# Kernel optimization log

Hardware: AMD Instinct MI355X
Metric: run time of the kernel (lower is better)

The kernel has to match this reference:

```python
import jax, jax.numpy as jnp
import numpy as np

N = 100000  # nodes per type (user, tweet)
E = 500000  # edges per relation
D = 128     # input feature dim
H = 128     # hidden dim


def _seg_mean(h_src, src, dst, n_dst):
    # DGL copy_u + mean: mean of source features over incoming edges; zero for in-degree 0.
    msg = h_src[src]                                                    # [E, F] gather
    s = jax.ops.segment_sum(msg, dst, num_segments=n_dst)               # [n_dst, F] scatter-add
    cnt = jax.ops.segment_sum(jnp.ones((src.shape[0], 1), h_src.dtype), dst, num_segments=n_dst)
    return s / jnp.maximum(cnt, 1.0)


def setup_inputs() -> dict:
    key = jax.random.key(0)
    ks = jax.random.split(key, 24)
    f = lambda i, shp, s=1.0: jax.random.normal(ks[i], shp, dtype=jnp.float32) * s
    return {
        'x_user': f(0, (N, D)), 'x_tweet': f(1, (N, D)),
        # layer 1, relation 'posts' (user -> tweet) and 'posted_by' (tweet -> user)
        'w1ps': f(2, (H, D), 0.05), 'b1ps': f(3, (H,), 0.05),
        'w1pn': f(4, (H, D), 0.05), 'b1pn': f(5, (H,), 0.05),
        'w1bs': f(6, (H, D), 0.05), 'b1bs': f(7, (H,), 0.05),
        'w1bn': f(8, (H, D), 0.05), 'b1bn': f(9, (H,), 0.05),
        # layer 2 (out_feats = 1, no activation)
        'w2ps': f(10, (1, H), 0.05), 'b2ps': f(11, (1,), 0.05),
        'w2pn': f(12, (1, H), 0.05), 'b2pn': f(13, (1,), 0.05),
        'w2bs': f(14, (1, H), 0.05), 'b2bs': f(15, (1,), 0.05),
        'w2bn': f(16, (1, H), 0.05), 'b2bn': f(17, (1,), 0.05),
        'src_posts': jax.random.randint(ks[18], (E,), 0, N),
        'dst_posts': jax.random.randint(ks[19], (E,), 0, N),
        'src_pb': jax.random.randint(ks[20], (E,), 0, N),
        'dst_pb': jax.random.randint(ks[21], (E,), 0, N),
    }


def reference(x_user, x_tweet,
              w1ps, b1ps, w1pn, b1pn, w1bs, b1bs, w1bn, b1bn,
              w2ps, b2ps, w2pn, b2pn, w2bs, b2bs, w2bn, b2bn,
              src_posts, dst_posts, src_pb, dst_pb):
    # ---- conv1: DivFeatConv per relation, relu, cross-relation sum (one rel per dst type) ----
    neigh_t = _seg_mean(x_user, src_posts, dst_posts, N)               # user -posts-> tweet
    h_tweet = jax.nn.relu(x_tweet @ w1ps.T + b1ps + neigh_t @ w1pn.T + b1pn)
    neigh_u = _seg_mean(x_tweet, src_pb, dst_pb, N)                    # tweet -posted_by-> user
    h_user = jax.nn.relu(x_user @ w1bs.T + b1bs + neigh_u @ w1bn.T + b1bn)
    # ---- conv2: out_feats=1, identity activation ----
    neigh_t2 = _seg_mean(h_user, src_posts, dst_posts, N)
    out_tweet = h_tweet @ w2ps.T + b2ps + neigh_t2 @ w2pn.T + b2pn     # [N, 1]
    neigh_u2 = _seg_mean(h_tweet, src_pb, dst_pb, N)
    out_user = h_user @ w2bs.T + b2bs + neigh_u2 @ w2bn.T + b2bn       # [N, 1]
    return (out_user, out_tweet)
```

## Files before the change

kernel.cpp:

```cpp
#include <hip/hip_runtime.h>

#define N_NODES 100000
#define N_EDGES 500000
#define DIM 128
#define GB_E 1954
#define GB_EI 489
#define GB_N 391
#define GB_CVT 12500
#define GB_G 782
#define GB_SEG 6250

typedef __attribute__((ext_vector_type(8))) short short8;
typedef __attribute__((ext_vector_type(4))) float f32x4;

__device__ __forceinline__ ushort f2bf(float f) {
    unsigned u = __float_as_uint(f);
    u += 0x7FFF + ((u >> 16) & 1);
    return (ushort)(u >> 16);
}
__device__ __forceinline__ float bf2f(ushort s) {
    return __uint_as_float(((unsigned)s) << 16);
}


__device__ __forceinline__ void build_body(const int* __restrict__ src,
                                           const int* __restrict__ dst,
                                           int* __restrict__ head,
                                           int2* __restrict__ entry, int bid) {
    int e = bid * 256 + threadIdx.x;
    if (e < N_EDGES) {
        int d = dst[e];
        int old = atomicExch(&head[d], e);
        entry[e] = make_int2(src[e], old);
    }
}

__device__ __forceinline__ void build_body_ilp(const int* __restrict__ src,
                                               const int* __restrict__ dst,
                                               int* __restrict__ head,
                                               int2* __restrict__ entry, int bid) {
    int base = bid * 1024 + threadIdx.x;
    int e[4], d[4], s[4], old[4];
    bool ok[4];
#pragma unroll
    for (int k = 0; k < 4; ++k) {
        e[k] = base + k * 256;
        ok[k] = (e[k] < N_EDGES);
        d[k] = ok[k] ? dst[e[k]] : 0;
        s[k] = ok[k] ? src[e[k]] : 0;
    }
#pragma unroll
    for (int k = 0; k < 4; ++k)
        if (ok[k]) old[k] = atomicExch(&head[d[k]], e[k]);
#pragma unroll
    for (int k = 0; k < 4; ++k)
        if (ok[k]) entry[e[k]] = make_int2(s[k], old[k]);
}

__device__ __forceinline__ void cvt_body(const float* __restrict__ in,
                                         ushort* __restrict__ out, int bid) {
    int i = (bid * 256 + threadIdx.x) * 4;
    float4 v = *reinterpret_cast<const float4*>(&in[i]);
    ushort4 u = make_ushort4(f2bf(v.x), f2bf(v.y), f2bf(v.z), f2bf(v.w));
    *reinterpret_cast<ushort4*>(&out[i]) = u;
}

__device__ __forceinline__ void seg_body(const ushort* __restrict__ x,
                                         const int* __restrict__ head,
                                         const int2* __restrict__ entry,
                                         ushort* __restrict__ outbf, int bid) {
    int idx = bid * 256 + threadIdx.x;
    int node = idx >> 4;
    if (node >= N_NODES) return;
    int f = (idx & 15) << 3;
    float acc[8];
#pragma unroll
    for (int j = 0; j < 8; ++j) acc[j] = 0.f;
    int cnt = 0;
    int e = head[node];
    while (e >= 0) {
        int2 nd = entry[e];
        ++cnt;
        short8 v = *reinterpret_cast<const short8*>(&x[(size_t)nd.x * DIM + f]);
#pragma unroll
        for (int j = 0; j < 8; ++j) acc[j] += bf2f((ushort)v[j]);
        e = nd.y;
    }
    float r = 1.0f / fmaxf((float)cnt, 1.0f);
    union { ushort s[8]; uint4 v; } u;
#pragma unroll
    for (int j = 0; j < 8; ++j) u.s[j] = f2bf(acc[j] * r);
    *reinterpret_cast<uint4*>(&outbf[(size_t)node * DIM + f]) = u.v;
}

__device__ __forceinline__ float smean_body(const float* __restrict__ sval,
                                            const int* __restrict__ head,
                                            const int2* __restrict__ entry, int node) {
    float a = 0.f;
    int cnt = 0;
    int e = head[node];
    while (e >= 0) {
        int2 nd = entry[e];
        ++cnt;
        a += sval[nd.x];
        e = nd.y;
    }
    return a / fmaxf((float)cnt, 1.0f);
}

__device__ __forceinline__ void gemm_body(
    const ushort* __restrict__ Xsbf, const ushort* __restrict__ Nm,
    const ushort* __restrict__ Wsbf, const ushort* __restrict__ Wnbf,
    const float* __restrict__ bs, const float* __restrict__ bn,
    const float* __restrict__ w2a, const float* __restrict__ w2b,
    float* __restrict__ dself, float* __restrict__ dcross, int blk) {
    __shared__ ushort sA[128 * 64];
    __shared__ ushort sB[128 * 64];
    __shared__ float pS[2][2][128];

    const int tid = threadIdx.x;
    const int lane = tid & 63;
    const int wid = tid >> 6;
    const int wr = wid >> 1, wc = wid & 1;
    const int lr = lane & 15, lg = lane >> 4;
    const int row0 = blk * 128;

    f32x4 acc[4][4];
#pragma unroll
    for (int i = 0; i < 4; ++i)
#pragma unroll
        for (int j = 0; j < 4; ++j) acc[i][j] = (f32x4){0.f, 0.f, 0.f, 0.f};

    const int r = tid >> 1;
    const int hh = tid & 1;
    const int grow = row0 + r;
    const int swzr = (r & 7) << 4;

    for (int kb = 0; kb < 256; kb += 64) {
        const int kg = kb & 127;
        const bool self = (kb < 128);
        __syncthreads();
        {
            const uint4* g = reinterpret_cast<const uint4*>(self ? Xsbf : Nm);
#pragma unroll
            for (int q = 0; q < 4; ++q) {
                uint4 v = make_uint4(0, 0, 0, 0);
                if (grow < N_NODES)
                    v = g[((size_t)grow * DIM + kg + hh * 32 + q * 8) >> 3];
                int byte = (hh * 64 + q * 16) ^ swzr;
                *reinterpret_cast<uint4*>(&sA[r * 64 + (byte >> 1)]) = v;
            }
        }
        {
            const uint4* g = reinterpret_cast<const uint4*>(self ? Wsbf : Wnbf);
#pragma unroll
            for (int q = 0; q < 4; ++q) {
                uint4 v = g[(r * DIM + kg + hh * 32 + q * 8) >> 3];
                int byte = (hh * 64 + q * 16) ^ swzr;
                *reinterpret_cast<uint4*>(&sB[r * 64 + (byte >> 1)]) = v;
            }
        }
        __syncthreads();
#pragma unroll
        for (int ks = 0; ks < 2; ++ks) {
            short8 a[4], b[4];
#pragma unroll
            for (int fm = 0; fm < 4; ++fm) {
                int rr = wr * 64 + fm * 16 + lr;
                int byte = (ks * 64 + lg * 16) ^ ((rr & 7) << 4);
                a[fm] = *reinterpret_cast<const short8*>(&sA[rr * 64 + (byte >> 1)]);
            }
#pragma unroll
            for (int fn = 0; fn < 4; ++fn) {
                int cc = wc * 64 + fn * 16 + lr;
                int byte = (ks * 64 + lg * 16) ^ ((cc & 7) << 4);
                b[fn] = *reinterpret_cast<const short8*>(&sB[cc * 64 + (byte >> 1)]);
            }
#pragma unroll
            for (int fm = 0; fm < 4; ++fm)
#pragma unroll
                for (int fn = 0; fn < 4; ++fn)
                    acc[fm][fn] = __builtin_amdgcn_mfma_f32_16x16x32_bf16(
                        a[fm], b[fn], acc[fm][fn], 0, 0, 0);
        }
    }

    float bias[4], wa[4], wb[4];
#pragma unroll
    for (int fn = 0; fn < 4; ++fn) {
        int c = wc * 64 + fn * 16 + lr;
        bias[fn] = bs[c] + bn[c];
        wa[fn] = w2a[c];
        wb[fn] = w2b[c];
    }
#pragma unroll
    for (int fm = 0; fm < 4; ++fm) {
#pragma unroll
        for (int reg = 0; reg < 4; ++reg) {
            float pa = 0.f, pb = 0.f;
#pragma unroll
            for (int fn = 0; fn < 4; ++fn) {
                float h = fmaxf(acc[fm][fn][reg] + bias[fn], 0.f);
                pa = fmaf(h, wa[fn], pa);
                pb = fmaf(h, wb[fn], pb);
            }
#pragma unroll
            for (int m = 1; m < 16; m <<= 1) {
                pa += __shfl_xor(pa, m);
                pb += __shfl_xor(pb, m);
            }
            if (lr == 0) {
                int rloc = wr * 64 + fm * 16 + lg * 4 + reg;
                pS[wc][0][rloc] = pa;
                pS[wc][1][rloc] = pb;
            }
        }
    }
    __syncthreads();
    if (tid < 128) {
        int go = row0 + tid;
        if (go < N_NODES) {
            dself[go] = pS[0][0][tid] + pS[1][0][tid];
            dcross[go] = pS[0][1][tid] + pS[1][1][tid];
        }
    }
}


__global__ __launch_bounds__(256) void cvt_fat_kernel(
    const float* __restrict__ w0, const float* __restrict__ w1,
    const float* __restrict__ w2, const float* __restrict__ w3,
    ushort* __restrict__ o0, ushort* __restrict__ o1,
    ushort* __restrict__ o2, ushort* __restrict__ o3,
    const float* __restrict__ xu, const float* __restrict__ xt,
    ushort* __restrict__ xbf_u, ushort* __restrict__ xbf_t) {
    int bid = blockIdx.x;
    if (bid < 64) {
        int a = bid >> 4;
        const float* in = (a == 0) ? w0 : (a == 1) ? w1 : (a == 2) ? w2 : w3;
        ushort* out = (a == 0) ? o0 : (a == 1) ? o1 : (a == 2) ? o2 : o3;
        cvt_body(in, out, bid & 15);
    } else {
        int b = bid - 64;
        int which = (b >= GB_CVT);
        cvt_body(which ? xt : xu, which ? xbf_t : xbf_u, b - which * GB_CVT);
    }
}

__global__ __launch_bounds__(256) void build1_ilp_kernel(
    const int* __restrict__ src, const int* __restrict__ dst,
    int* __restrict__ head, int2* __restrict__ entry) {
    build_body_ilp(src, dst, head, entry, blockIdx.x);
}

__global__ __launch_bounds__(256) void seg_only_kernel(
    const ushort* __restrict__ x, const int* __restrict__ head,
    const int2* __restrict__ entry, ushort* __restrict__ outbf) {
    seg_body(x, head, entry, outbf, blockIdx.x);
}

__global__ __launch_bounds__(256) void fatG_kernel(
    const ushort* __restrict__ xbf_t, const ushort* __restrict__ nbf0,
    const ushort* __restrict__ wbf_ps, const ushort* __restrict__ wbf_pn,
    const float* __restrict__ b1ps, const float* __restrict__ b1pn,
    const float* __restrict__ w2ps, const float* __restrict__ w2bn,
    float* __restrict__ dself_t, float* __restrict__ scross_t,
    const int* __restrict__ s1, const int* __restrict__ d1,
    int* __restrict__ head_pb, int2* __restrict__ ent_pb) {
    int bid = blockIdx.x;
    if (bid < GB_G)
        gemm_body(xbf_t, nbf0, wbf_ps, wbf_pn, b1ps, b1pn, w2ps, w2bn,
                  dself_t, scross_t, bid);
    else
        build_body_ilp(s1, d1, head_pb, ent_pb, bid - GB_G);
}

__global__ __launch_bounds__(256) void fatC_kernel(
    const ushort* __restrict__ xbf_u, const ushort* __restrict__ nbf1,
    const ushort* __restrict__ wbf_bs, const ushort* __restrict__ wbf_bn,
    const float* __restrict__ b1bs, const float* __restrict__ b1bn,
    const float* __restrict__ w2bs, const float* __restrict__ w2pn,
    float* __restrict__ dself_u, float* __restrict__ scross_u,
    const float* __restrict__ scross_t,
    const int* __restrict__ head_pb, const int2* __restrict__ ent_pb,
    float* __restrict__ smean_u) {
    int bid = blockIdx.x;
    if (bid < GB_G) {
        gemm_body(xbf_u, nbf1, wbf_bs, wbf_bn, b1bs, b1bn, w2bs, w2pn,
                  dself_u, scross_u, bid);
    } else {
        int i = (bid - GB_G) * 256 + threadIdx.x;
        if (i < N_NODES) smean_u[i] = smean_body(scross_t, head_pb, ent_pb, i);
    }
}

__global__ __launch_bounds__(256) void tail_kernel(
    const float* __restrict__ dself_u, const float* __restrict__ smean_u,
    const float* __restrict__ dself_t, const float* __restrict__ scross_u,
    const int* __restrict__ head_posts, const int2* __restrict__ ent_posts,
    const float* __restrict__ b2bs, const float* __restrict__ b2bn,
    const float* __restrict__ b2ps, const float* __restrict__ b2pn,
    float* __restrict__ out) {
    int i = blockIdx.x * 256 + threadIdx.x;
    if (i >= N_NODES) return;
    out[N_NODES + i] = dself_t[i] + smean_body(scross_u, head_posts, ent_posts, i)
                       + b2ps[0] + b2pn[0];
    out[i] = dself_u[i] + smean_u[i] + b2bs[0] + b2bn[0];
}


__global__ __launch_bounds__(256) void cvtw_kernel(
    const float* __restrict__ w0, const float* __restrict__ w1,
    const float* __restrict__ w2, const float* __restrict__ w3,
    ushort* __restrict__ o0, ushort* __restrict__ o1,
    ushort* __restrict__ o2, ushort* __restrict__ o3) {
    int a = blockIdx.y;
    const float* in = (a == 0) ? w0 : (a == 1) ? w1 : (a == 2) ? w2 : w3;
    ushort* out = (a == 0) ? o0 : (a == 1) ? o1 : (a == 2) ? o2 : o3;
    cvt_body(in, out, blockIdx.x);
}

__global__ __launch_bounds__(256) void build_lists2_kernel(
    const int* __restrict__ s0, const int* __restrict__ d0,
    const int* __restrict__ s1, const int* __restrict__ d1,
    int* __restrict__ head2, int2* __restrict__ entry2) {
    const int rel = blockIdx.y;
    build_body(rel ? s1 : s0, rel ? d1 : d0, head2 + (size_t)rel * N_NODES,
               entry2 + (size_t)rel * N_EDGES, blockIdx.x);
}

__global__ __launch_bounds__(256) void seg_mean_f32_list_kernel(
    const float* __restrict__ x, const int* __restrict__ head,
    const int2* __restrict__ entry, ushort* __restrict__ outbf) {
    int idx = blockIdx.x * 256 + threadIdx.x;
    int node = idx >> 5;
    if (node >= N_NODES) return;
    int f = (idx & 31) << 2;
    float4 acc = make_float4(0.f, 0.f, 0.f, 0.f);
    int cnt = 0;
    int e = head[node];
    while (e >= 0) {
        int2 nd = entry[e];
        ++cnt;
        float4 v = *reinterpret_cast<const float4*>(&x[(size_t)nd.x * DIM + f]);
        acc.x += v.x; acc.y += v.y; acc.z += v.z; acc.w += v.w;
        e = nd.y;
    }
    float r = 1.0f / fmaxf((float)cnt, 1.0f);
    ushort4 u = make_ushort4(f2bf(acc.x * r), f2bf(acc.y * r),
                             f2bf(acc.z * r), f2bf(acc.w * r));
    *reinterpret_cast<ushort4*>(&outbf[node * DIM + f]) = u;
}

__global__ __launch_bounds__(256) void gemm_mfma_f32_kernel(
    const float* __restrict__ Xs, const ushort* __restrict__ Nm,
    const ushort* __restrict__ Wsbf, const ushort* __restrict__ Wnbf,
    const float* __restrict__ bs, const float* __restrict__ bn,
    const float* __restrict__ w2a, const float* __restrict__ w2b,
    float* __restrict__ dself, float* __restrict__ dcross) {
    __shared__ ushort sA[128 * 64];
    __shared__ ushort sB[128 * 64];
    __shared__ float pS[2][2][128];

    const int tid = threadIdx.x;
    const int lane = tid & 63;
    const int wid = tid >> 6;
    const int wr = wid >> 1, wc = wid & 1;
    const int lr = lane & 15, lg = lane >> 4;
    const int row0 = blockIdx.x * 128;

    f32x4 acc[4][4];
#pragma unroll
    for (int i = 0; i < 4; ++i)
#pragma unroll
        for (int j = 0; j < 4; ++j) acc[i][j] = (f32x4){0.f, 0.f, 0.f, 0.f};

    const int r = tid >> 1;
    const int hh = tid & 1;
    const int grow = row0 + r;
    const int swzr = (r & 7) << 4;

    for (int kb = 0; kb < 256; kb += 64) {
        const int kg = kb & 127;
        const bool self = (kb < 128);
        __syncthreads();
        if (self) {
            const float4* g = reinterpret_cast<const float4*>(Xs);
#pragma unroll
            for (int q = 0; q < 4; ++q) {
                float4 v0 = make_float4(0.f, 0.f, 0.f, 0.f), v1 = v0;
                if (grow < N_NODES) {
                    size_t bi = ((size_t)grow * DIM + kg + hh * 32 + q * 8) >> 2;
                    v0 = g[bi];
                    v1 = g[bi + 1];
                }
                union { ushort s[8]; uint4 v; } u;
                u.s[0] = f2bf(v0.x); u.s[1] = f2bf(v0.y);
                u.s[2] = f2bf(v0.z); u.s[3] = f2bf(v0.w);
                u.s[4] = f2bf(v1.x); u.s[5] = f2bf(v1.y);
                u.s[6] = f2bf(v1.z); u.s[7] = f2bf(v1.w);
                int byte = (hh * 64 + q * 16) ^ swzr;
                *reinterpret_cast<uint4*>(&sA[r * 64 + (byte >> 1)]) = u.v;
            }
        } else {
            const uint4* g = reinterpret_cast<const uint4*>(Nm);
#pragma unroll
            for (int q = 0; q < 4; ++q) {
                uint4 v = make_uint4(0, 0, 0, 0);
                if (grow < N_NODES)
                    v = g[((size_t)grow * DIM + kg + hh * 32 + q * 8) >> 3];
                int byte = (hh * 64 + q * 16) ^ swzr;
                *reinterpret_cast<uint4*>(&sA[r * 64 + (byte >> 1)]) = v;
            }
        }
        {
            const uint4* g = reinterpret_cast<const uint4*>(self ? Wsbf : Wnbf);
#pragma unroll
            for (int q = 0; q < 4; ++q) {
                uint4 v = g[(r * DIM + kg + hh * 32 + q * 8) >> 3];
                int byte = (hh * 64 + q * 16) ^ swzr;
                *reinterpret_cast<uint4*>(&sB[r * 64 + (byte >> 1)]) = v;
            }
        }
        __syncthreads();
#pragma unroll
        for (int ks = 0; ks < 2; ++ks) {
            short8 a[4], b[4];
#pragma unroll
            for (int fm = 0; fm < 4; ++fm) {
                int rr = wr * 64 + fm * 16 + lr;
                int byte = (ks * 64 + lg * 16) ^ ((rr & 7) << 4);
                a[fm] = *reinterpret_cast<const short8*>(&sA[rr * 64 + (byte >> 1)]);
            }
#pragma unroll
            for (int fn = 0; fn < 4; ++fn) {
                int cc = wc * 64 + fn * 16 + lr;
                int byte = (ks * 64 + lg * 16) ^ ((cc & 7) << 4);
                b[fn] = *reinterpret_cast<const short8*>(&sB[cc * 64 + (byte >> 1)]);
            }
#pragma unroll
            for (int fm = 0; fm < 4; ++fm)
#pragma unroll
                for (int fn = 0; fn < 4; ++fn)
                    acc[fm][fn] = __builtin_amdgcn_mfma_f32_16x16x32_bf16(
                        a[fm], b[fn], acc[fm][fn], 0, 0, 0);
        }
    }

    float bias[4], wa[4], wb[4];
#pragma unroll
    for (int fn = 0; fn < 4; ++fn) {
        int c = wc * 64 + fn * 16 + lr;
        bias[fn] = bs[c] + bn[c];
        wa[fn] = w2a[c];
        wb[fn] = w2b[c];
    }
#pragma unroll
    for (int fm = 0; fm < 4; ++fm) {
#pragma unroll
        for (int reg = 0; reg < 4; ++reg) {
            float pa = 0.f, pb = 0.f;
#pragma unroll
            for (int fn = 0; fn < 4; ++fn) {
                float h = fmaxf(acc[fm][fn][reg] + bias[fn], 0.f);
                pa = fmaf(h, wa[fn], pa);
                pb = fmaf(h, wb[fn], pb);
            }
#pragma unroll
            for (int m = 1; m < 16; m <<= 1) {
                pa += __shfl_xor(pa, m);
                pb += __shfl_xor(pb, m);
            }
            if (lr == 0) {
                int rloc = wr * 64 + fm * 16 + lg * 4 + reg;
                pS[wc][0][rloc] = pa;
                pS[wc][1][rloc] = pb;
            }
        }
    }
    __syncthreads();
    if (tid < 128) {
        int go = row0 + tid;
        if (go < N_NODES) {
            dself[go] = pS[0][0][tid] + pS[1][0][tid];
            dcross[go] = pS[0][1][tid] + pS[1][1][tid];
        }
    }
}

__global__ __launch_bounds__(256) void scalar_finalize_kernel(
    const float* __restrict__ dself_u, const float* __restrict__ dself_t,
    const float* __restrict__ scross_u, const float* __restrict__ scross_t,
    const int* __restrict__ head2, const int2* __restrict__ entry2,
    const float* __restrict__ b2bs, const float* __restrict__ b2bn,
    const float* __restrict__ b2ps, const float* __restrict__ b2pn,
    float* __restrict__ out) {
    int i = blockIdx.x * 256 + threadIdx.x;
    if (i >= N_NODES) return;
    out[N_NODES + i] = dself_t[i] + smean_body(scross_u, head2, entry2, i)
                       + b2ps[0] + b2pn[0];
    out[i] = dself_u[i] + smean_body(scross_t, head2 + N_NODES, entry2 + N_EDGES, i)
             + b2bs[0] + b2bn[0];
}


extern "C" void kernel_launch(void* const* d_in, const int* in_sizes, int n_in,
                              void* d_out, int out_size, void* d_ws, size_t ws_size,
                              hipStream_t stream) {
    const float* x_user  = (const float*)d_in[0];
    const float* x_tweet = (const float*)d_in[1];
    const float* w1ps = (const float*)d_in[2];  const float* b1ps = (const float*)d_in[3];
    const float* w1pn = (const float*)d_in[4];  const float* b1pn = (const float*)d_in[5];
    const float* w1bs = (const float*)d_in[6];  const float* b1bs = (const float*)d_in[7];
    const float* w1bn = (const float*)d_in[8];  const float* b1bn = (const float*)d_in[9];
    const float* w2ps = (const float*)d_in[10]; const float* b2ps = (const float*)d_in[11];
    const float* w2pn = (const float*)d_in[12]; const float* b2pn = (const float*)d_in[13];
    const float* w2bs = (const float*)d_in[14]; const float* b2bs = (const float*)d_in[15];
    const float* w2bn = (const float*)d_in[16]; const float* b2bn = (const float*)d_in[17];
    const int* src_posts = (const int*)d_in[18];
    const int* dst_posts = (const int*)d_in[19];
    const int* src_pb    = (const int*)d_in[20];
    const int* dst_pb    = (const int*)d_in[21];
    float* out = (float*)d_out;

    char* wsb = (char*)d_ws;
    ushort* nbf0    = (ushort*)wsb;   wsb += (size_t)N_NODES * DIM * 2;
    int* head2      = (int*)wsb;      wsb += (size_t)2 * N_NODES * 4;
    int2* entry2    = (int2*)wsb;     wsb += (size_t)2 * N_EDGES * 8;
    ushort* wbf_ps  = (ushort*)wsb;   wsb += (size_t)DIM * DIM * 2;
    ushort* wbf_pn  = (ushort*)wsb;   wsb += (size_t)DIM * DIM * 2;
    ushort* wbf_bs  = (ushort*)wsb;   wsb += (size_t)DIM * DIM * 2;
    ushort* wbf_bn  = (ushort*)wsb;   wsb += (size_t)DIM * DIM * 2;
    float* dself_t  = (float*)wsb;    wsb += (size_t)N_NODES * 4;
    float* scross_t = (float*)wsb;    wsb += (size_t)N_NODES * 4;
    float* dself_u  = (float*)wsb;    wsb += (size_t)N_NODES * 4;
    float* scross_u = (float*)wsb;    wsb += (size_t)N_NODES * 4;
    float* smean_u  = (float*)wsb;    wsb += (size_t)N_NODES * 4;
    ushort* nbf1    = (ushort*)wsb;   wsb += (size_t)N_NODES * DIM * 2;
    ushort* xbf_u   = (ushort*)wsb;   wsb += (size_t)N_NODES * DIM * 2;
    ushort* xbf_t   = (ushort*)wsb;   wsb += (size_t)N_NODES * DIM * 2;
    const bool use_bf = ((size_t)(wsb - (char*)d_ws) <= ws_size);

    int* head_posts = head2;
    int* head_pb    = head2 + N_NODES;
    int2* ent_posts = entry2;
    int2* ent_pb    = entry2 + N_EDGES;

    hipMemsetAsync(head2, 0xFF, (size_t)2 * N_NODES * sizeof(int), stream);

    if (!use_bf) {
        cvtw_kernel<<<dim3(16, 4), 256, 0, stream>>>(w1ps, w1pn, w1bs, w1bn,
                                                     wbf_ps, wbf_pn, wbf_bs, wbf_bn);
        build_lists2_kernel<<<dim3(GB_E, 2), 256, 0, stream>>>(
            src_posts, dst_posts, src_pb, dst_pb, head2, entry2);
        seg_mean_f32_list_kernel<<<(N_NODES * 32 + 255) / 256, 256, 0, stream>>>(
            x_user, head_posts, ent_posts, nbf0);
        gemm_mfma_f32_kernel<<<GB_G, 256, 0, stream>>>(x_tweet, nbf0, wbf_ps, wbf_pn,
                                                       b1ps, b1pn, w2ps, w2bn,
                                                       dself_t, scross_t);
        seg_mean_f32_list_kernel<<<(N_NODES * 32 + 255) / 256, 256, 0, stream>>>(
            x_tweet, head_pb, ent_pb, nbf0);
        gemm_mfma_f32_kernel<<<GB_G, 256, 0, stream>>>(x_user, nbf0, wbf_bs, wbf_bn,
                                                       b1bs, b1bn, w2bs, w2pn,
                                                       dself_u, scross_u);
        scalar_finalize_kernel<<<GB_N, 256, 0, stream>>>(dself_u, dself_t,
                                                         scross_u, scross_t,
                                                         head2, entry2,
                                                         b2bs, b2bn, b2ps, b2pn, out);
        return;
    }

    cvt_fat_kernel<<<64 + 2 * GB_CVT, 256, 0, stream>>>(
        w1ps, w1pn, w1bs, w1bn, wbf_ps, wbf_pn, wbf_bs, wbf_bn,
        x_user, x_tweet, xbf_u, xbf_t);

    build1_ilp_kernel<<<GB_EI, 256, 0, stream>>>(src_posts, dst_posts,
                                                 head_posts, ent_posts);

    seg_only_kernel<<<GB_SEG, 256, 0, stream>>>(xbf_u, head_posts, ent_posts, nbf0);

    fatG_kernel<<<GB_G + GB_EI, 256, 0, stream>>>(
        xbf_t, nbf0, wbf_ps, wbf_pn, b1ps, b1pn, w2ps, w2bn,
        dself_t, scross_t, src_pb, dst_pb, head_pb, ent_pb);

    seg_only_kernel<<<GB_SEG, 256, 0, stream>>>(xbf_t, head_pb, ent_pb, nbf1);

    fatC_kernel<<<GB_G + GB_N, 256, 0, stream>>>(
        xbf_u, nbf1, wbf_bs, wbf_bn, b1bs, b1bn, w2bs, w2pn,
        dself_u, scross_u, scross_t, head_pb, ent_pb, smean_u);

    tail_kernel<<<GB_N, 256, 0, stream>>>(dself_u, smean_u, dself_t, scross_u,
                                          head_posts, ent_posts,
                                          b2bs, b2bn, b2ps, b2pn, out);
}
```

Before: 197.5 us.

## Batch both relations into 2D-grid build, segment-mean, and GEMM kernels

New measurement: 188.4 us (median of 2 runs). -4.6%, faster.

```diff
diff --git a/kernel.cpp b/kernel.cpp
--- a/kernel.cpp
+++ b/kernel.cpp
@@ -247,65 +247,58 @@
     }
 }
 
-__global__ __launch_bounds__(256) void build1_ilp_kernel(
-    const int* __restrict__ src, const int* __restrict__ dst,
-    int* __restrict__ head, int2* __restrict__ entry) {
-    build_body_ilp(src, dst, head, entry, blockIdx.x);
-}
-
-__global__ __launch_bounds__(256) void seg_only_kernel(
-    const ushort* __restrict__ x, const int* __restrict__ head,
-    const int2* __restrict__ entry, ushort* __restrict__ outbf) {
-    seg_body(x, head, entry, outbf, blockIdx.x);
-}
-
-__global__ __launch_bounds__(256) void fatG_kernel(
+__global__ __launch_bounds__(256) void build2_ilp_kernel(
+    const int* __restrict__ s0, const int* __restrict__ d0,
+    const int* __restrict__ s1, const int* __restrict__ d1,
+    int* __restrict__ head2, int2* __restrict__ entry2) {
+    const int rel = blockIdx.y;
+    build_body_ilp(rel ? s1 : s0, rel ? d1 : d0, head2 + (size_t)rel * N_NODES,
+                   entry2 + (size_t)rel * N_EDGES, blockIdx.x);
+}
+
+__global__ __launch_bounds__(256) void seg2_kernel(
+    const ushort* __restrict__ xbf_u, const int* __restrict__ head_posts,
+    const int2* __restrict__ ent_posts, ushort* __restrict__ nbf0,
+    const ushort* __restrict__ xbf_t, const int* __restrict__ head_pb,
+    const int2* __restrict__ ent_pb, ushort* __restrict__ nbf1) {
+    if (blockIdx.y == 0)
+        seg_body(xbf_u, head_posts, ent_posts, nbf0, blockIdx.x);
+    else
+        seg_body(xbf_t, head_pb, ent_pb, nbf1, blockIdx.x);
+}
+
+__global__ __launch_bounds__(256) void gemm2_kernel(
     const ushort* __restrict__ xbf_t, const ushort* __restrict__ nbf0,
     const ushort* __restrict__ wbf_ps, const ushort* __restrict__ wbf_pn,
     const float* __restrict__ b1ps, const float* __restrict__ b1pn,
     const float* __restrict__ w2ps, const float* __restrict__ w2bn,
     float* __restrict__ dself_t, float* __restrict__ scross_t,
-    const int* __restrict__ s1, const int* __restrict__ d1,
-    int* __restrict__ head_pb, int2* __restrict__ ent_pb) {
-    int bid = blockIdx.x;
-    if (bid < GB_G)
-        gemm_body(xbf_t, nbf0, wbf_ps, wbf_pn, b1ps, b1pn, w2ps, w2bn,
-                  dself_t, scross_t, bid);
-    else
-        build_body_ilp(s1, d1, head_pb, ent_pb, bid - GB_G);
-}
-
-__global__ __launch_bounds__(256) void fatC_kernel(
     const ushort* __restrict__ xbf_u, const ushort* __restrict__ nbf1,
     const ushort* __restrict__ wbf_bs, const ushort* __restrict__ wbf_bn,
     const float* __restrict__ b1bs, const float* __restrict__ b1bn,
     const float* __restrict__ w2bs, const float* __restrict__ w2pn,
-    float* __restrict__ dself_u, float* __restrict__ scross_u,
-    const float* __restrict__ scross_t,
-    const int* __restrict__ head_pb, const int2* __restrict__ ent_pb,
-    float* __restrict__ smean_u) {
-    int bid = blockIdx.x;
-    if (bid < GB_G) {
+    float* __restrict__ dself_u, float* __restrict__ scross_u) {
+    if (blockIdx.y == 0)
+        gemm_body(xbf_t, nbf0, wbf_ps, wbf_pn, b1ps, b1pn, w2ps, w2bn,
+                  dself_t, scross_t, blockIdx.x);
+    else
         gemm_body(xbf_u, nbf1, wbf_bs, wbf_bn, b1bs, b1bn, w2bs, w2pn,
-                  dself_u, scross_u, bid);
-    } else {
-        int i = (bid - GB_G) * 256 + threadIdx.x;
-        if (i < N_NODES) smean_u[i] = smean_body(scross_t, head_pb, ent_pb, i);
-    }
-}
-
-__global__ __launch_bounds__(256) void tail_kernel(
-    const float* __restrict__ dself_u, const float* __restrict__ smean_u,
-    const float* __restrict__ dself_t, const float* __restrict__ scross_u,
-    const int* __restrict__ head_posts, const int2* __restrict__ ent_posts,
+                  dself_u, scross_u, blockIdx.x);
+}
+
+__global__ __launch_bounds__(256) void scalar_finalize_kernel(
+    const float* __restrict__ dself_u, const float* __restrict__ dself_t,
+    const float* __restrict__ scross_u, const float* __restrict__ scross_t,
+    const int* __restrict__ head2, const int2* __restrict__ entry2,
     const float* __restrict__ b2bs, const float* __restrict__ b2bn,
     const float* __restrict__ b2ps, const float* __restrict__ b2pn,
     float* __restrict__ out) {
     int i = blockIdx.x * 256 + threadIdx.x;
     if (i >= N_NODES) return;
-    out[N_NODES + i] = dself_t[i] + smean_body(scross_u, head_posts, ent_posts, i)
+    out[N_NODES + i] = dself_t[i] + smean_body(scross_u, head2, entry2, i)
                        + b2ps[0] + b2pn[0];
-    out[i] = dself_u[i] + smean_u[i] + b2bs[0] + b2bn[0];
+    out[i] = dself_u[i] + smean_body(scross_t, head2 + N_NODES, entry2 + N_EDGES, i)
+             + b2bs[0] + b2bn[0];
 }
 
 
@@ -486,21 +479,6 @@
             dcross[go] = pS[0][1][tid] + pS[1][1][tid];
         }
     }
-}
-
-__global__ __launch_bounds__(256) void scalar_finalize_kernel(
-    const float* __restrict__ dself_u, const float* __restrict__ dself_t,
-    const float* __restrict__ scross_u, const float* __restrict__ scross_t,
-    const int* __restrict__ head2, const int2* __restrict__ entry2,
-    const float* __restrict__ b2bs, const float* __restrict__ b2bn,
-    const float* __restrict__ b2ps, const float* __restrict__ b2pn,
-    float* __restrict__ out) {
-    int i = blockIdx.x * 256 + threadIdx.x;
-    if (i >= N_NODES) return;
-    out[N_NODES + i] = dself_t[i] + smean_body(scross_u, head2, entry2, i)
-                       + b2ps[0] + b2pn[0];
-    out[i] = dself_u[i] + smean_body(scross_t, head2 + N_NODES, entry2 + N_EDGES, i)
-             + b2bs[0] + b2bn[0];
 }
 
 
@@ -574,22 +552,18 @@
         w1ps, w1pn, w1bs, w1bn, wbf_ps, wbf_pn, wbf_bs, wbf_bn,
         x_user, x_tweet, xbf_u, xbf_t);
 
-    build1_ilp_kernel<<<GB_EI, 256, 0, stream>>>(src_posts, dst_posts,
-                                                 head_posts, ent_posts);
-
-    seg_only_kernel<<<GB_SEG, 256, 0, stream>>>(xbf_u, head_posts, ent_posts, nbf0);
-
-    fatG_kernel<<<GB_G + GB_EI, 256, 0, stream>>>(
-        xbf_t, nbf0, wbf_ps, wbf_pn, b1ps, b1pn, w2ps, w2bn,
-        dself_t, scross_t, src_pb, dst_pb, head_pb, ent_pb);
-
-    seg_only_kernel<<<GB_SEG, 256, 0, stream>>>(xbf_t, head_pb, ent_pb, nbf1);
-
-    fatC_kernel<<<GB_G + GB_N, 256, 0, stream>>>(
-        xbf_u, nbf1, wbf_bs, wbf_bn, b1bs, b1bn, w2bs, w2pn,
-        dself_u, scross_u, scross_t, head_pb, ent_pb, smean_u);
-
-    tail_kernel<<<GB_N, 256, 0, stream>>>(dself_u, smean_u, dself_t, scross_u,
-                                          head_posts, ent_posts,
-                                          b2bs, b2bn, b2ps, b2pn, out);
-}
+    build2_ilp_kernel<<<dim3(GB_EI, 2), 256, 0, stream>>>(
+        src_posts, dst_posts, src_pb, dst_pb, head2, entry2);
+
+    seg2_kernel<<<dim3(GB_SEG, 2), 256, 0, stream>>>(
+        xbf_u, head_posts, ent_posts, nbf0, xbf_t, head_pb, ent_pb, nbf1);
+
+    gemm2_kernel<<<dim3(GB_G, 2), 256, 0, stream>>>(
+        xbf_t, nbf0, wbf_ps, wbf_pn, b1ps, b1pn, w2ps, w2bn, dself_t, scross_t,
+        xbf_u, nbf1, wbf_bs, wbf_bn, b1bs, b1bn, w2bs, w2pn, dself_u, scross_u);
+
+    scalar_finalize_kernel<<<GB_N, 256, 0, stream>>>(dself_u, dself_t,
+                                                     scross_u, scross_t,
+                                                     head2, entry2,
+                                                     b2bs, b2bn, b2ps, b2pn, out);
+}
```
